# Kernel optimization log

Hardware: AMD Instinct MI355X
Metric: run time of the kernel (lower is better)

Reference implementation:

```python
import jax, jax.numpy as jnp
import numpy as np

CH = 64
CF = CH // 8  # f/g projection channels


def setup_inputs() -> dict:
    key = jax.random.key(0)
    k1, k2, k3, k4, k5 = jax.random.split(key, 5)
    x = jax.random.normal(k1, (8, 64, 64, CH), dtype=jnp.float32)
    kernel_f = 0.02 * jax.random.normal(k2, (1, 1, CH, CF), dtype=jnp.float32)
    kernel_g = 0.02 * jax.random.normal(k3, (1, 1, CH, CF), dtype=jnp.float32)
    kernel_h = 0.02 * jax.random.normal(k4, (1, 1, CH, CH), dtype=jnp.float32)
    gamma = 0.02 * jax.random.normal(k5, (1,), dtype=jnp.float32)
    return {"x": x, "kernel_f": kernel_f, "kernel_g": kernel_g,
            "kernel_h": kernel_h, "gamma": gamma}


def reference(x, kernel_f, kernel_g, kernel_h, gamma):
    B, H, W, C = x.shape
    N = H * W
    xf = x.reshape(B, N, C)  # flatten spatial; 1x1 conv == matmul over channels
    f = jnp.einsum('bnc,cd->bnd', xf, kernel_f[0, 0])  # [B,N,CF]
    g = jnp.einsum('bnc,cd->bnd', xf, kernel_g[0, 0])  # [B,N,CF]
    h = jnp.einsum('bnc,cd->bnd', xf, kernel_h[0, 0])  # [B,N,C]
    s = jnp.einsum('bnd,bmd->bnm', g, f)  # g @ f^T, [B,N,N]
    beta = jax.nn.softmax(s, axis=-1)
    o = jnp.einsum('bnm,bmc->bnc', beta, h)  # [B,N,C]
    out = gamma * o.reshape(B, H, W, C) + x
    return out
```

## Files before the change

kernel.cpp:

```cpp
#include <hip/hip_runtime.h>
#include <hip/hip_bf16.h>

typedef __attribute__((ext_vector_type(4)))  float f32x4;
typedef __attribute__((ext_vector_type(16))) float f32x16;
typedef __attribute__((ext_vector_type(8)))  short bf16x8;

#define LOG2E 1.44269504088896340736f

#if __has_builtin(__builtin_amdgcn_exp2f)
static __device__ __forceinline__ float exp2_native(float x) {
  return __builtin_amdgcn_exp2f(x);
}
#else
extern "C" __device__ float __ocml_native_exp2_f32(float);
static __device__ __forceinline__ float exp2_native(float x) {
  return __ocml_native_exp2_f32(x);
}
#endif

static __device__ __forceinline__ unsigned int pack_trunc_f(float a, float b) {
  return __builtin_amdgcn_perm(__float_as_uint(b), __float_as_uint(a), 0x07060302);
}

typedef const __attribute__((address_space(1))) unsigned int gu32;
typedef __attribute__((address_space(3))) unsigned int lu32;
static __device__ __forceinline__ void gload_lds16(const void* g, void* l) {
  __builtin_amdgcn_global_load_lds((gu32*)g, (lu32*)l, 16, 0, 0);
}

__global__ __launch_bounds__(256) void proj_kernel(
    const float* __restrict__ x, const float* __restrict__ kf,
    const float* __restrict__ kg, const float* __restrict__ kh,
    unsigned short* __restrict__ f_b, unsigned short* __restrict__ g_b,
    unsigned short* __restrict__ h_p)
{
  __shared__ unsigned short Kt[80*72];
  const int t = threadIdx.x;
  const int idb = blockIdx.x;
  const int blk = (idb & 7)*64 + (idb >> 3);

  #pragma unroll
  for (int r = 0; r < 20; ++r) {
    int idx = r*256 + t;
    int o = idx >> 6, c = idx & 63;
    float v = (o < 8) ? kf[c*8 + o]
            : (o < 16) ? kg[c*8 + (o-8)] * LOG2E
            : kh[c*64 + (o-16)];
    Kt[o*72 + c] = (unsigned short)(__float_as_uint(v) >> 16);
  }
  __syncthreads();

  const int w = t >> 6, lane = t & 63, l15 = lane & 15, quad = lane >> 4;
  const int Rbase = blk*64 + w*16;
  const int R = Rbase + l15;

  bf16x8 af[2];
  #pragma unroll
  for (int kk = 0; kk < 2; ++kk) {
    const float* xp = x + (long)R*64 + kk*32 + quad*8;
    float4 v0 = *(const float4*)xp;
    float4 v1 = *(const float4*)(xp + 4);
    union { unsigned int u[4]; bf16x8 v; } p;
    p.u[0] = pack_trunc_f(v0.x, v0.y);
    p.u[1] = pack_trunc_f(v0.z, v0.w);
    p.u[2] = pack_trunc_f(v1.x, v1.y);
    p.u[3] = pack_trunc_f(v1.z, v1.w);
    af[kk] = p.v;
  }

  f32x4 acc[5];
  #pragma unroll
  for (int nt = 0; nt < 5; ++nt) { f32x4 z = {}; acc[nt] = z; }

  #pragma unroll
  for (int nt = 0; nt < 5; ++nt)
    #pragma unroll
    for (int kk = 0; kk < 2; ++kk) {
      bf16x8 bfv = *(const bf16x8*)&Kt[(nt*16 + l15)*72 + kk*32 + quad*8];
      acc[nt] = __builtin_amdgcn_mfma_f32_16x16x32_bf16(af[kk], bfv, acc[nt], 0, 0, 0);
    }

  const int bt = Rbase >> 12;
  const int kt = (Rbase >> 7) & 31;
  const int base = ((blk & 1) << 6) + (w << 4);
  const int pi = base + ((quad & 1) << 3) + (((quad >> 1) & 1) << 2);

  #pragma unroll
  for (int rr = 0; rr < 4; ++rr) {
    const int nq = (Rbase + quad*4 + rr) & 4095;
    unsigned short v = (unsigned short)(__float_as_uint(acc[0][rr]) >> 16);
    if (l15 < 8) f_b[((long)bt*4096 + nq)*8 + l15] = v;
    else         g_b[((long)bt*4096 + nq)*8 + (l15 - 8)] = v;
  }
  #pragma unroll
  for (int nt = 1; nt < 5; ++nt) {
    const int c = (nt - 1)*16 + l15;
    uint2 v;
    v.x = pack_trunc_f(acc[nt][0], acc[nt][1]);
    v.y = pack_trunc_f(acc[nt][2], acc[nt][3]);
    *(uint2*)(h_p + ((long)(bt*32 + kt)*64 + c)*136 + pi) = v;
  }
}

__global__ __launch_bounds__(1024, 4) void attn_kernel(
    const unsigned short* __restrict__ f_b, const unsigned short* __restrict__ g_b,
    const unsigned short* __restrict__ h_p,
    const float* __restrict__ x, const float* __restrict__ gamma_p,
    float* __restrict__ out)
{
  extern __shared__ char smem[];

  const int t = threadIdx.x;
  const int w = t >> 6, lane = t & 63, l31 = lane & 31, a = lane >> 5;
  const int qg = w & 3, ks = w >> 2;
  const int id = blockIdx.x;
  const int b = id & 7, qb = id >> 3;
  const int q0 = qb*128 + qg*32;

  bf16x8 gfv;
  {
    bf16x8 gv = *(const bf16x8*)(g_b + ((long)b*4096 + q0 + l31)*8);
    bf16x8 z = {};
    gfv = (a == 0) ? gv : z;
  }
  bf16x8 bhl;
  {
    union { unsigned short s[8]; bf16x8 v; } o8;
    #pragma unroll
    for (int j = 0; j < 8; ++j) o8.s[j] = 0x3F80;
    bf16x8 z = {};
    bhl = (l31 == 0) ? o8.v : z;
  }

  f32x16 oacc[2], ol;
  { f32x16 z = {}; oacc[0] = z; oacc[1] = z; ol = z; }

  const char* hp_b = (const char*)h_p + (long)b*32*17408;
  const char* fb_b = (const char*)f_b + (long)b*4096*16;

  auto stage = [&](int bi, int tp) {
    char* dst = smem + bi*38912;
    #pragma unroll
    for (int i = 0; i < 3; ++i) {
      const int c = i*16 + w;
      if (c < 38) {
        const int off = c*1024;
        const int sub = (off >= 19456);
        const int kt = tp*2 + sub;
        const int within = off - sub*19456;
        const char* src = (within < 17408)
            ? (hp_b + (long)kt*17408 + within)
            : (fb_b + (long)kt*2048 + (within - 17408));
        gload_lds16(src + lane*16, dst + off);
      }
    }
  };

  stage(0, 0);

  for (int tp = 0; tp < 16; ++tp) {
    __syncthreads();
    if (tp < 15) stage((tp + 1) & 1, tp + 1);

    const char* bufb = smem + (tp & 1)*38912;

    #pragma unroll
    for (int sub = 0; sub < 2; ++sub) {
      const unsigned short* hts = (const unsigned short*)(bufb + sub*19456);
      const unsigned short* fts = hts + 8704;

      bf16x8 afv = *(const bf16x8*)&fts[(ks*32 + l31)*8];
      f32x16 zz = {};
      f32x16 sc = __builtin_amdgcn_mfma_f32_32x32x16_bf16(afv, gfv, zz, 0, 0, 0);

      #pragma unroll
      for (int half = 0; half < 2; ++half) {
        const int s = ks*2 + half;
        bf16x8 bh0 = *(const bf16x8*)&hts[(l31)*136      + s*16 + a*8];
        bf16x8 bh1 = *(const bf16x8*)&hts[(32 + l31)*136 + s*16 + a*8];
        union { unsigned int u[4]; bf16x8 v; } ap;
        #pragma unroll
        for (int j = 0; j < 4; ++j) {
          float ea = exp2_native(sc[half*8 + 2*j]);
          float eb = exp2_native(sc[half*8 + 2*j + 1]);
          ap.u[j] = pack_trunc_f(ea, eb);
        }
        oacc[0] = __builtin_amdgcn_mfma_f32_32x32x16_bf16(ap.v, bh0, oacc[0], 0, 0, 0);
        oacc[1] = __builtin_amdgcn_mfma_f32_32x32x16_bf16(ap.v, bh1, oacc[1], 0, 0, 0);
        ol      = __builtin_amdgcn_mfma_f32_32x32x16_bf16(ap.v, bhl, ol,      0, 0, 0);
      }
    }
  }

  __syncthreads();
  float* cb = (float*)smem;
  #pragma unroll
  for (int rnd = 0; rnd < 2; ++rnd) {
    if ((qg >> 1) == rnd && ks > 0) {
      float* d = cb + (((qg & 1)*3 + (ks - 1))*64 + lane)*49;
      #pragma unroll
      for (int r = 0; r < 16; ++r) {
        d[r] = oacc[0][r]; d[16 + r] = oacc[1][r]; d[32 + r] = ol[r];
      }
    }
    __syncthreads();
    if ((qg >> 1) == rnd && ks == 0) {
      #pragma unroll
      for (int sl = 0; sl < 3; ++sl) {
        const float* sp = cb + (((qg & 1)*3 + sl)*64 + lane)*49;
        #pragma unroll
        for (int r = 0; r < 16; ++r) {
          oacc[0][r] += sp[r]; oacc[1][r] += sp[16 + r]; ol[r] += sp[32 + r];
        }
      }
    }
    __syncthreads();
  }

  if (ks == 0) {
    const float gamma = gamma_p[0];
    const float* xb = x + ((long)b*4096 + q0)*64;
    float* ob = out + ((long)b*4096 + q0)*64;

    #pragma unroll
    for (int r = 0; r < 16; ++r) {
      const int q = (r & 3) + 8*(r >> 2) + 4*a;
      const float lq = __shfl(ol[r], lane & 32);
      const float s = gamma / lq;
      #pragma unroll
      for (int nt = 0; nt < 2; ++nt) {
        const long idx = (long)q*64 + nt*32 + l31;
        ob[idx] = fmaf(s, oacc[nt][r], xb[idx]);
      }
    }
  }
}

extern "C" void kernel_launch(void* const* d_in, const int* in_sizes, int n_in,
                              void* d_out, int out_size, void* d_ws, size_t ws_size,
                              hipStream_t stream) {
  const float* x  = (const float*)d_in[0];
  const float* kf = (const float*)d_in[1];
  const float* kg = (const float*)d_in[2];
  const float* kh = (const float*)d_in[3];
  const float* gamma = (const float*)d_in[4];
  float* out = (float*)d_out;

  char* ws = (char*)d_ws;
  unsigned short* h_p = (unsigned short*)ws;
  unsigned short* f_b = (unsigned short*)(ws + 4456448);
  unsigned short* g_b = (unsigned short*)(ws + 4980736);

  proj_kernel<<<512, 256, 0, stream>>>(x, kf, kg, kh, f_b, g_b, h_p);
  attn_kernel<<<256, 1024, 77824, stream>>>(f_b, g_b, h_p, x, gamma, out);
}
```

Before: 102.9 us.

## Give each attention wave two query groups and halve block size

The attention kernel moves from 1024-thread blocks (4 query groups × 4 key splits) to 512-thread blocks. Each wave now handles two 32-query groups against one key sub-tile, so every f and h fragment read from LDS feeds twice as many MFMAs. Blocks cover 64 queries, so the grid doubles to 512 and each block still stages the full key/value stream. The cross-wave reduction becomes a three-round combine into wave 0. The cost is twice the accumulator registers per wave and twice the total global-to-LDS staging traffic across blocks.

```diff
diff --git a/kernel.cpp b/kernel.cpp
--- a/kernel.cpp
+++ b/kernel.cpp
@@ -102,7 +102,7 @@
   }
 }
 
-__global__ __launch_bounds__(1024, 4) void attn_kernel(
+__global__ __launch_bounds__(512, 2) void attn_kernel(
     const unsigned short* __restrict__ f_b, const unsigned short* __restrict__ g_b,
     const unsigned short* __restrict__ h_p,
     const float* __restrict__ x, const float* __restrict__ gamma_p,
@@ -112,16 +112,17 @@
 
   const int t = threadIdx.x;
   const int w = t >> 6, lane = t & 63, l31 = lane & 31, a = lane >> 5;
-  const int qg = w & 3, ks = w >> 2;
+  const int tl = w >> 2, mt = w & 3;
   const int id = blockIdx.x;
   const int b = id & 7, qb = id >> 3;
-  const int q0 = qb*128 + qg*32;
-
-  bf16x8 gfv;
-  {
-    bf16x8 gv = *(const bf16x8*)(g_b + ((long)b*4096 + q0 + l31)*8);
+  const int q0 = qb*64;
+
+  bf16x8 gf[2];
+  #pragma unroll
+  for (int qg = 0; qg < 2; ++qg) {
+    bf16x8 gv = *(const bf16x8*)(g_b + ((long)b*4096 + q0 + qg*32 + l31)*8);
     bf16x8 z = {};
-    gfv = (a == 0) ? gv : z;
+    gf[qg] = (a == 0) ? gv : z;
   }
   bf16x8 bhl;
   {
@@ -132,8 +133,10 @@
     bhl = (l31 == 0) ? o8.v : z;
   }
 
-  f32x16 oacc[2], ol;
-  { f32x16 z = {}; oacc[0] = z; oacc[1] = z; ol = z; }
+  f32x16 oacc[2][2], ol[2];
+  { f32x16 z = {};
+    oacc[0][0] = z; oacc[0][1] = z; oacc[1][0] = z; oacc[1][1] = z;
+    ol[0] = z; ol[1] = z; }
 
   const char* hp_b = (const char*)h_p + (long)b*32*17408;
   const char* fb_b = (const char*)f_b + (long)b*4096*16;
@@ -141,8 +144,8 @@
   auto stage = [&](int bi, int tp) {
     char* dst = smem + bi*38912;
     #pragma unroll
-    for (int i = 0; i < 3; ++i) {
-      const int c = i*16 + w;
+    for (int i = 0; i < 5; ++i) {
+      const int c = i*8 + w;
       if (c < 38) {
         const int off = c*1024;
         const int sub = (off >= 19456);
@@ -163,74 +166,88 @@
     if (tp < 15) stage((tp + 1) & 1, tp + 1);
 
     const char* bufb = smem + (tp & 1)*38912;
-
-    #pragma unroll
-    for (int sub = 0; sub < 2; ++sub) {
-      const unsigned short* hts = (const unsigned short*)(bufb + sub*19456);
-      const unsigned short* fts = hts + 8704;
-
-      bf16x8 afv = *(const bf16x8*)&fts[(ks*32 + l31)*8];
-      f32x16 zz = {};
-      f32x16 sc = __builtin_amdgcn_mfma_f32_32x32x16_bf16(afv, gfv, zz, 0, 0, 0);
-
+    const unsigned short* hts = (const unsigned short*)(bufb + tl*19456);
+    const unsigned short* fts = hts + 8704;
+
+    bf16x8 afv = *(const bf16x8*)&fts[(mt*32 + l31)*8];
+    f32x16 zz = {};
+    f32x16 sc0 = __builtin_amdgcn_mfma_f32_32x32x16_bf16(afv, gf[0], zz, 0, 0, 0);
+    f32x16 sc1 = __builtin_amdgcn_mfma_f32_32x32x16_bf16(afv, gf[1], zz, 0, 0, 0);
+
+    #pragma unroll
+    for (int half = 0; half < 2; ++half) {
+      const int s = mt*2 + half;
+      bf16x8 bh0 = *(const bf16x8*)&hts[(l31)*136      + s*16 + a*8];
+      bf16x8 bh1 = *(const bf16x8*)&hts[(32 + l31)*136 + s*16 + a*8];
+      union { unsigned int u[4]; bf16x8 v; } ap0, ap1;
       #pragma unroll
-      for (int half = 0; half < 2; ++half) {
-        const int s = ks*2 + half;
-        bf16x8 bh0 = *(const bf16x8*)&hts[(l31)*136      + s*16 + a*8];
-        bf16x8 bh1 = *(const bf16x8*)&hts[(32 + l31)*136 + s*16 + a*8];
-        union { unsigned int u[4]; bf16x8 v; } ap;
-        #pragma unroll
-        for (int j = 0; j < 4; ++j) {
-          float ea = exp2_native(sc[half*8 + 2*j]);
-          float eb = exp2_native(sc[half*8 + 2*j + 1]);
-          ap.u[j] = pack_trunc_f(ea, eb);
-        }
-        oacc[0] = __builtin_amdgcn_mfma_f32_32x32x16_bf16(ap.v, bh0, oacc[0], 0, 0, 0);
-        oacc[1] = __builtin_amdgcn_mfma_f32_32x32x16_bf16(ap.v, bh1, oacc[1], 0, 0, 0);
-        ol      = __builtin_amdgcn_mfma_f32_32x32x16_bf16(ap.v, bhl, ol,      0, 0, 0);
-      }
+      for (int j = 0; j < 4; ++j) {
+        float e0a = exp2_native(sc0[half*8 + 2*j]);
+        float e0b = exp2_native(sc0[half*8 + 2*j + 1]);
+        float e1a = exp2_native(sc1[half*8 + 2*j]);
+        float e1b = exp2_native(sc1[half*8 + 2*j + 1]);
+        ap0.u[j] = pack_trunc_f(e0a, e0b);
+        ap1.u[j] = pack_trunc_f(e1a, e1b);
+      }
+      oacc[0][0] = __builtin_amdgcn_mfma_f32_32x32x16_bf16(ap0.v, bh0, oacc[0][0], 0, 0, 0);
+      oacc[0][1] = __builtin_amdgcn_mfma_f32_32x32x16_bf16(ap0.v, bh1, oacc[0][1], 0, 0, 0);
+      ol[0]      = __builtin_amdgcn_mfma_f32_32x32x16_bf16(ap0.v, bhl, ol[0],      0, 0, 0);
+      oacc[1][0] = __builtin_amdgcn_mfma_f32_32x32x16_bf16(ap1.v, bh0, oacc[1][0], 0, 0, 0);
+      oacc[1][1] = __builtin_amdgcn_mfma_f32_32x32x16_bf16(ap1.v, bh1, oacc[1][1], 0, 0, 0);
+      ol[1]      = __builtin_amdgcn_mfma_f32_32x32x16_bf16(ap1.v, bhl, ol[1],      0, 0, 0);
     }
   }
 
   __syncthreads();
   float* cb = (float*)smem;
   #pragma unroll
-  for (int rnd = 0; rnd < 2; ++rnd) {
-    if ((qg >> 1) == rnd && ks > 0) {
-      float* d = cb + (((qg & 1)*3 + (ks - 1))*64 + lane)*49;
+  for (int rnd = 0; rnd < 3; ++rnd) {
+    const int lo = rnd*3 + 1;
+    if (w >= lo && w < lo + 3) {
+      #pragma unroll
+      for (int qg = 0; qg < 2; ++qg) {
+        float* d = cb + (((w - lo)*2 + qg)*64 + lane)*49;
+        #pragma unroll
+        for (int r = 0; r < 16; ++r) {
+          d[r] = oacc[qg][0][r]; d[16 + r] = oacc[qg][1][r]; d[32 + r] = ol[qg][r];
+        }
+      }
+    }
+    __syncthreads();
+    if (w == 0) {
+      const int nsl = (rnd == 2) ? 1 : 3;
+      for (int sl = 0; sl < nsl; ++sl) {
+        #pragma unroll
+        for (int qg = 0; qg < 2; ++qg) {
+          const float* sp = cb + ((sl*2 + qg)*64 + lane)*49;
+          #pragma unroll
+          for (int r = 0; r < 16; ++r) {
+            oacc[qg][0][r] += sp[r];
+            oacc[qg][1][r] += sp[16 + r];
+            ol[qg][r]      += sp[32 + r];
+          }
+        }
+      }
+    }
+    __syncthreads();
+  }
+
+  if (w == 0) {
+    const float gamma = gamma_p[0];
+    #pragma unroll
+    for (int qg = 0; qg < 2; ++qg) {
+      const float* xb = x + ((long)b*4096 + q0 + qg*32)*64;
+      float* ob = out + ((long)b*4096 + q0 + qg*32)*64;
       #pragma unroll
       for (int r = 0; r < 16; ++r) {
-        d[r] = oacc[0][r]; d[16 + r] = oacc[1][r]; d[32 + r] = ol[r];
-      }
-    }
-    __syncthreads();
-    if ((qg >> 1) == rnd && ks == 0) {
-      #pragma unroll
-      for (int sl = 0; sl < 3; ++sl) {
-        const float* sp = cb + (((qg & 1)*3 + sl)*64 + lane)*49;
+        const int q = (r & 3) + 8*(r >> 2) + 4*a;
+        const float lq = __shfl(ol[qg][r], lane & 32);
+        const float s = gamma / lq;
         #pragma unroll
-        for (int r = 0; r < 16; ++r) {
-          oacc[0][r] += sp[r]; oacc[1][r] += sp[16 + r]; ol[r] += sp[32 + r];
+        for (int nt = 0; nt < 2; ++nt) {
+          const long idx = (long)q*64 + nt*32 + l31;
+          ob[idx] = fmaf(s, oacc[qg][nt][r], xb[idx]);
         }
-      }
-    }
-    __syncthreads();
-  }
-
-  if (ks == 0) {
-    const float gamma = gamma_p[0];
-    const float* xb = x + ((long)b*4096 + q0)*64;
-    float* ob = out + ((long)b*4096 + q0)*64;
-
-    #pragma unroll
-    for (int r = 0; r < 16; ++r) {
-      const int q = (r & 3) + 8*(r >> 2) + 4*a;
-      const float lq = __shfl(ol[r], lane & 32);
-      const float s = gamma / lq;
-      #pragma unroll
-      for (int nt = 0; nt < 2; ++nt) {
-        const long idx = (long)q*64 + nt*32 + l31;
-        ob[idx] = fmaf(s, oacc[nt][r], xb[idx]);
       }
     }
   }
@@ -252,5 +269,5 @@
   unsigned short* g_b = (unsigned short*)(ws + 4980736);
 
   proj_kernel<<<512, 256, 0, stream>>>(x, kf, kg, kh, f_b, g_b, h_p);
-  attn_kernel<<<256, 1024, 77824, stream>>>(f_b, g_b, h_p, x, gamma, out);
-}
+  attn_kernel<<<512, 512, 77824, stream>>>(f_b, g_b, h_p, x, gamma, out);
+}
```

Result: slower. 116.3 us (+13.0%).
